# Optimization experiments

Hardware: AMD Instinct MI355X
Metric: run time of the kernel (lower is better)

The kernel has to match this reference:

```python
import jax, jax.numpy as jnp
import numpy as np

B, S, D, H = 2, 2048, 1024, 16
Dh = D // H
LN_EPS = 1e-5


def setup_inputs() -> dict:
    key = jax.random.key(0)
    ks = jax.random.split(key, 14)
    s = 1.0 / np.sqrt(D)
    return {
        "q": jax.random.normal(ks[0], (B, S, D), jnp.float32),
        "k": jax.random.normal(ks[1], (B, S, D), jnp.float32),
        "v": jax.random.normal(ks[2], (B, S, D), jnp.float32),
        "attn_mask": jax.random.randint(ks[3], (B, S, S), 0, 2).astype(bool),
        "Wq": jax.random.normal(ks[4], (D, D), jnp.float32) * s,
        "bq": jnp.zeros((D,), jnp.float32),
        "Wk": jax.random.normal(ks[5], (D, D), jnp.float32) * s,
        "bk": jnp.zeros((D,), jnp.float32),
        "Wv": jax.random.normal(ks[6], (D, D), jnp.float32) * s,
        "bv": jnp.zeros((D,), jnp.float32),
        "Wo": jax.random.normal(ks[7], (D, D), jnp.float32) * s,
        "bo": jnp.zeros((D,), jnp.float32),
        "gamma": jnp.ones((D,), jnp.float32),
        "beta": jnp.zeros((D,), jnp.float32),
    }


def reference(q, k, v, attn_mask, Wq, bq, Wk, bk, Wv, bv, Wo, bo, gamma, beta):
    residual = q
    # projections (W stored as [in, out])
    qh = (q @ Wq + bq).reshape(B, S, H, Dh).transpose(0, 2, 1, 3)  # [B,H,S,Dh]
    kh = (k @ Wk + bk).reshape(B, S, H, Dh).transpose(0, 2, 1, 3)
    vh = (v @ Wv + bv).reshape(B, S, H, Dh).transpose(0, 2, 1, 3)
    scores = jnp.einsum("bhqd,bhkd->bhqk", qh, kh) / np.sqrt(Dh)
    scores = jnp.where(attn_mask[:, None, :, :], -1e9, scores)
    attn = jax.nn.softmax(scores, axis=-1)  # dropout is identity in eval
    context = jnp.einsum("bhqk,bhkd->bhqd", attn, vh)  # [B,H,S,Dh]
    # faithful to original bug: flat reshape WITHOUT transposing heads back
    context = context.reshape(B, S, D)
    out = context @ Wo + bo
    x = residual + out
    mu = jnp.mean(x, axis=-1, keepdims=True)
    var = jnp.var(x, axis=-1, keepdims=True)
    out = (x - mu) / jnp.sqrt(var + LN_EPS) * gamma + beta
    return out, attn
```

## Files before the change

### kernel.cpp

```cpp
#include <hip/hip_runtime.h>
#include <hip/hip_bf16.h>

typedef __attribute__((ext_vector_type(8))) short bf16x8;
typedef __attribute__((ext_vector_type(4))) float f32x4;

__device__ __forceinline__ short f2bf(float f) {
    union { float f; unsigned u; } v; v.f = f;
    unsigned r = (v.u + 0x7FFFu + ((v.u >> 16) & 1u)) >> 16;
    return (short)r;
}
__device__ __forceinline__ float bf2f(short s) {
    union { unsigned u; float f; } v; v.u = ((unsigned)(unsigned short)s) << 16;
    return v.f;
}
__device__ __forceinline__ void gll16(const void* g, void* l) {
    __builtin_amdgcn_global_load_lds(
        (const __attribute__((address_space(1))) unsigned int*)g,
        (__attribute__((address_space(3))) unsigned int*)l, 16, 0, 0);
}

__global__ __launch_bounds__(256) void k_cvt(const float* __restrict__ in, short* __restrict__ out) {
    const long i = ((long)blockIdx.x * 256 + threadIdx.x) * 8;
    float4 f0 = *reinterpret_cast<const float4*>(&in[i]);
    float4 f1 = *reinterpret_cast<const float4*>(&in[i + 4]);
    bf16x8 v;
    v[0] = f2bf(f0.x); v[1] = f2bf(f0.y); v[2] = f2bf(f0.z); v[3] = f2bf(f0.w);
    v[4] = f2bf(f1.x); v[5] = f2bf(f1.y); v[6] = f2bf(f1.z); v[7] = f2bf(f1.w);
    *reinterpret_cast<bf16x8*>(&out[i]) = v;
}

__global__ __launch_bounds__(256) void k_wt(const float* __restrict__ W, short* __restrict__ WT) {
    __shared__ float t[32][33];
    const int rb = blockIdx.y * 32, cb = blockIdx.x * 32;
    const int tr = threadIdx.x >> 3, tc = (threadIdx.x & 7) * 4;
    const float4 v = *reinterpret_cast<const float4*>(&W[(long)(rb + tr) * 1024 + cb + tc]);
    t[tr][tc + 0] = v.x; t[tr][tc + 1] = v.y; t[tr][tc + 2] = v.z; t[tr][tc + 3] = v.w;
    __syncthreads();
    short4 o;
    o.x = f2bf(t[tc + 0][tr]); o.y = f2bf(t[tc + 1][tr]);
    o.z = f2bf(t[tc + 2][tr]); o.w = f2bf(t[tc + 3][tr]);
    *reinterpret_cast<short4*>(&WT[(long)(cb + tr) * 1024 + rb + tc]) = o;
}

__global__ __launch_bounds__(256) void k_mask_bits(const int* __restrict__ mask, unsigned* __restrict__ bits) {
    __shared__ int sm[8192];
    const long base = (long)blockIdx.x * 8192;
    const int tid = threadIdx.x;
#pragma unroll
    for (int i = 0; i < 8; ++i) {
        *reinterpret_cast<int4*>(&sm[i * 1024 + tid * 4]) =
            *reinterpret_cast<const int4*>(&mask[base + i * 1024 + tid * 4]);
    }
    __syncthreads();
    unsigned wv = 0;
#pragma unroll
    for (int j = 0; j < 32; ++j) wv |= (sm[tid * 32 + j] != 0 ? 1u : 0u) << j;
    bits[base / 32 + tid] = wv;
}

template<int MODE>
__global__ __launch_bounds__(256) void k_gemm2(
    const short* __restrict__ A, const short* __restrict__ BT,
    const float* __restrict__ bias, const float* __restrict__ resid,
    void* __restrict__ outp, float scale)
{
    __shared__ short As[128 * 64];
    __shared__ short Bs[128 * 64];
    const int tid = threadIdx.x, w = tid >> 6, lane = tid & 63;
    const int lr = lane & 15, lg = lane >> 4;
    const int rowbase = blockIdx.y * 128, colbase = blockIdx.x * 128;
    const int wr = (w >> 1) * 64, wc = (w & 1) * 64;
    const int srow = lane >> 3, sc_ = (lane & 7) ^ srow;

    f32x4 acc[4][4] = {};

    for (int kb = 0; kb < 1024; kb += 64) {
#pragma unroll
        for (int ii = 0; ii < 4; ++ii) {
            const int rl = w * 32 + ii * 8 + srow;
            gll16(A + (long)(rowbase + rl) * 1024 + kb + sc_ * 8, &As[(w * 32 + ii * 8) * 64]);
            gll16(BT + (long)(colbase + rl) * 1024 + kb + sc_ * 8, &Bs[(w * 32 + ii * 8) * 64]);
        }
        __syncthreads();
#pragma unroll
        for (int ks = 0; ks < 2; ++ks) {
            bf16x8 a[4], bq[4];
#pragma unroll
            for (int m = 0; m < 4; ++m) {
                const int r = wr + m * 16 + lr;
                a[m] = *reinterpret_cast<const bf16x8*>(&As[r * 64 + (((ks * 4 + lg) ^ (r & 7)) << 3)]);
            }
#pragma unroll
            for (int n = 0; n < 4; ++n) {
                const int r = wc + n * 16 + lr;
                bq[n] = *reinterpret_cast<const bf16x8*>(&Bs[r * 64 + (((ks * 4 + lg) ^ (r & 7)) << 3)]);
            }
#pragma unroll
            for (int m = 0; m < 4; ++m)
#pragma unroll
                for (int n = 0; n < 4; ++n)
                    acc[m][n] = __builtin_amdgcn_mfma_f32_16x16x32_bf16(a[m], bq[n], acc[m][n], 0, 0, 0);
        }
        __syncthreads();
    }

#pragma unroll
    for (int m = 0; m < 4; ++m) {
#pragma unroll
        for (int n = 0; n < 4; ++n) {
            const int C = colbase + wc + n * 16 + lr;
            const float bv = bias[C];
#pragma unroll
            for (int rr = 0; rr < 4; ++rr) {
                const int R = rowbase + wr + m * 16 + lg * 4 + rr;
                float val = (acc[m][n][rr] + bv) * scale;
                if (MODE == 0) {
                    const int b = R >> 11, s = R & 2047, h = C >> 6, dh = C & 63;
                    ((short*)outp)[(((long)(b * 16 + h) * 2048 + s) << 6) + dh] = f2bf(val);
                } else if (MODE == 1) {
                    const int b = R >> 11, s = R & 2047, h = C >> 6, dh = C & 63;
                    ((short*)outp)[(((long)(b * 16 + h) * 64 + dh) << 11) + s] = f2bf(val);
                } else {
                    const long idx = (long)R * 1024 + C;
                    ((float*)outp)[idx] = val + resid[idx];
                }
            }
        }
    }
}

__global__ __launch_bounds__(256) void k_attn(
    const short* __restrict__ qh, const short* __restrict__ kh,
    const short* __restrict__ vt, const unsigned* __restrict__ mbits,
    float* __restrict__ attn_out, short* __restrict__ ctxb)
{
    const int bh = blockIdx.y, b = bh >> 4;
    const int tid = threadIdx.x, w = tid >> 6, lane = tid & 63;
    const int lr = lane & 15, lg = lane >> 4;
    const int ibase = blockIdx.x * 64 + w * 16;

    __shared__ short Ks[64 * 64];
    __shared__ short Vs[64 * 64];
    __shared__ short Ps[4][16 * 72];

    const short* qhp = qh + ((long)bh * 2048 + ibase) * 64;
    const short* khp = kh + (long)bh * 2048 * 64;
    const short* vtp = vt + (long)bh * 64 * 2048;
    const unsigned* mbp = mbits + (long)b * 2048 * 64 + (long)ibase * 64;

    const bf16x8 aq0 = *reinterpret_cast<const bf16x8*>(&qhp[lr * 64 + lg * 8]);
    const bf16x8 aq1 = *reinterpret_cast<const bf16x8*>(&qhp[lr * 64 + 32 + lg * 8]);

    const int srow = lane >> 3, sc_ = (lane & 7) ^ srow;

    auto stage_k = [&](int ch) {
#pragma unroll
        for (int ii = 0; ii < 2; ++ii) {
            const int rl = w * 16 + ii * 8 + srow;
            gll16(khp + (long)(ch * 64 + rl) * 64 + sc_ * 8, &Ks[(w * 16 + ii * 8) * 64]);
        }
    };
    auto stage_v = [&](int ch) {
#pragma unroll
        for (int ii = 0; ii < 2; ++ii) {
            const int rl = w * 16 + ii * 8 + srow;
            gll16(vtp + (long)rl * 2048 + ch * 64 + sc_ * 8, &Vs[(w * 16 + ii * 8) * 64]);
        }
    };
    auto kfrag = [&](int t, int ks) -> bf16x8 {
        const int r = t * 16 + lr;
        return *reinterpret_cast<const bf16x8*>(&Ks[r * 64 + (((ks * 4 + lg) ^ (r & 7)) << 3)]);
    };
    auto vfrag = [&](int g, int ks) -> bf16x8 {
        const int r = g * 16 + lr;
        return *reinterpret_cast<const bf16x8*>(&Vs[r * 64 + (((ks * 4 + lg) ^ (r & 7)) << 3)]);
    };

    float ml[4], ll[4];
#pragma unroll
    for (int rr = 0; rr < 4; ++rr) { ml[rr] = -3.0e38f; ll[rr] = 0.f; }

    for (int ch = 0; ch < 32; ++ch) {
        stage_k(ch);
        __syncthreads();
        unsigned mw[4][2];
#pragma unroll
        for (int rr = 0; rr < 4; ++rr)
#pragma unroll
            for (int h = 0; h < 2; ++h)
                mw[rr][h] = mbp[(lg * 4 + rr) * 64 + ch * 2 + h];
#pragma unroll
        for (int t = 0; t < 4; ++t) {
            f32x4 sc = {};
            sc = __builtin_amdgcn_mfma_f32_16x16x32_bf16(aq0, kfrag(t, 0), sc, 0, 0, 0);
            sc = __builtin_amdgcn_mfma_f32_16x16x32_bf16(aq1, kfrag(t, 1), sc, 0, 0, 0);
#pragma unroll
            for (int rr = 0; rr < 4; ++rr) {
                const bool masked = (mw[rr][t >> 1] >> (((t & 1) << 4) + lr)) & 1;
                const float s = masked ? -1e9f : sc[rr];
                const float d = s - ml[rr];
                const float e = __expf(-fabsf(d));
                const bool gt = d > 0.f;
                ll[rr] = gt ? ll[rr] * e + 1.f : ll[rr] + e;
                ml[rr] = gt ? s : ml[rr];
            }
        }
        __syncthreads();
    }

    float mf[4], il[4];
#pragma unroll
    for (int rr = 0; rr < 4; ++rr) {
        float mx = ml[rr];
#pragma unroll
        for (int off = 1; off < 16; off <<= 1) mx = fmaxf(mx, __shfl_xor(mx, off, 16));
        float lw = ll[rr] * __expf(ml[rr] - mx);
#pragma unroll
        for (int off = 1; off < 16; off <<= 1) lw += __shfl_xor(lw, off, 16);
        mf[rr] = mx; il[rr] = 1.0f / lw;
    }

    f32x4 accc[4] = {};
    const long arow0 = (long)bh * 2048 + ibase;

    for (int ch = 0; ch < 32; ++ch) {
        stage_k(ch);
        stage_v(ch);
        __syncthreads();
        unsigned mw[4][2];
#pragma unroll
        for (int rr = 0; rr < 4; ++rr)
#pragma unroll
            for (int h = 0; h < 2; ++h)
                mw[rr][h] = mbp[(lg * 4 + rr) * 64 + ch * 2 + h];
#pragma unroll
        for (int t = 0; t < 4; ++t) {
            f32x4 sc = {};
            sc = __builtin_amdgcn_mfma_f32_16x16x32_bf16(aq0, kfrag(t, 0), sc, 0, 0, 0);
            sc = __builtin_amdgcn_mfma_f32_16x16x32_bf16(aq1, kfrag(t, 1), sc, 0, 0, 0);
#pragma unroll
            for (int rr = 0; rr < 4; ++rr) {
                const bool masked = (mw[rr][t >> 1] >> (((t & 1) << 4) + lr)) & 1;
                const float s = masked ? -1e9f : sc[rr];
                const float p = __expf(s - mf[rr]) * il[rr];
                Ps[w][(lg * 4 + rr) * 72 + t * 16 + lr] = f2bf(p);
            }
        }
#pragma unroll
        for (int ks = 0; ks < 2; ++ks) {
            const bf16x8 pa = *reinterpret_cast<const bf16x8*>(&Ps[w][lr * 72 + ks * 32 + lg * 8]);
#pragma unroll
            for (int g = 0; g < 4; ++g)
                accc[g] = __builtin_amdgcn_mfma_f32_16x16x32_bf16(pa, vfrag(g, ks), accc[g], 0, 0, 0);
        }
#pragma unroll
        for (int i2 = 0; i2 < 4; ++i2) {
            const int r = i2 * 4 + lg;
            const short4 p4 = *reinterpret_cast<const short4*>(&Ps[w][r * 72 + lr * 4]);
            float4 o;
            o.x = bf2f(p4.x); o.y = bf2f(p4.y); o.z = bf2f(p4.z); o.w = bf2f(p4.w);
            *reinterpret_cast<float4*>(&attn_out[(arow0 + r) * 2048 + ch * 64 + lr * 4]) = o;
        }
        __syncthreads();
    }

#pragma unroll
    for (int g = 0; g < 4; ++g)
#pragma unroll
        for (int rr = 0; rr < 4; ++rr)
            ctxb[(arow0 + lg * 4 + rr) * 64 + g * 16 + lr] = f2bf(accc[g][rr]);
}

__global__ __launch_bounds__(256) void k_ln(const float* __restrict__ x,
    const float* __restrict__ gamma, const float* __restrict__ beta,
    float* __restrict__ out)
{
    __shared__ float red[8];
    const int r = blockIdx.x, tid = threadIdx.x;
    const float4 v = reinterpret_cast<const float4*>(x + (long)r * 1024)[tid];
    float s = v.x + v.y + v.z + v.w;
    float q2 = v.x * v.x + v.y * v.y + v.z * v.z + v.w * v.w;
#pragma unroll
    for (int off = 32; off; off >>= 1) {
        s += __shfl_xor(s, off, 64);
        q2 += __shfl_xor(q2, off, 64);
    }
    if ((tid & 63) == 0) { red[(tid >> 6) * 2] = s; red[(tid >> 6) * 2 + 1] = q2; }
    __syncthreads();
    s = red[0] + red[2] + red[4] + red[6];
    q2 = red[1] + red[3] + red[5] + red[7];
    const float mu = s * (1.0f / 1024.0f);
    const float var = q2 * (1.0f / 1024.0f) - mu * mu;
    const float rs = rsqrtf(var + 1e-5f);
    const float4 g = reinterpret_cast<const float4*>(gamma)[tid];
    const float4 bb = reinterpret_cast<const float4*>(beta)[tid];
    float4 o;
    o.x = (v.x - mu) * rs * g.x + bb.x;
    o.y = (v.y - mu) * rs * g.y + bb.y;
    o.z = (v.z - mu) * rs * g.z + bb.z;
    o.w = (v.w - mu) * rs * g.w + bb.w;
    reinterpret_cast<float4*>(out + (long)r * 1024)[tid] = o;
}

extern "C" void kernel_launch(void* const* d_in, const int* in_sizes, int n_in,
                              void* d_out, int out_size, void* d_ws, size_t ws_size,
                              hipStream_t stream)
{
    const float* qin  = (const float*)d_in[0];
    const float* kin  = (const float*)d_in[1];
    const float* vin  = (const float*)d_in[2];
    const int*   mask = (const int*)d_in[3];
    const float* Wq = (const float*)d_in[4];
    const float* bq = (const float*)d_in[5];
    const float* Wk = (const float*)d_in[6];
    const float* bk = (const float*)d_in[7];
    const float* Wv = (const float*)d_in[8];
    const float* bv = (const float*)d_in[9];
    const float* Wo = (const float*)d_in[10];
    const float* bo = (const float*)d_in[11];
    const float* gamma = (const float*)d_in[12];
    const float* beta  = (const float*)d_in[13];

    char* ws = (char*)d_ws;
    short* WqT = (short*)(ws + (0ul  << 20));
    short* WkT = (short*)(ws + (2ul  << 20));
    short* WvT = (short*)(ws + (4ul  << 20));
    short* WoT = (short*)(ws + (6ul  << 20));
    short* qbf = (short*)(ws + (8ul  << 20));
    short* kbf = (short*)(ws + (16ul << 20));
    short* vbf = (short*)(ws + (24ul << 20));
    short* qh  = (short*)(ws + (32ul << 20));
    short* khb = (short*)(ws + (40ul << 20));
    short* vtb = (short*)(ws + (48ul << 20));
    unsigned* mb = (unsigned*)(ws + (56ul << 20));
    short* ctxb = (short*)(ws + (57ul << 20));
    float* xb   = (float*)(ws + (8ul  << 20));

    float* outLN = (float*)d_out;
    float* attnO = (float*)d_out + 4194304;

    const dim3 blk(256);
    k_cvt<<<dim3(2048), blk, 0, stream>>>(qin, qbf);
    k_cvt<<<dim3(2048), blk, 0, stream>>>(kin, kbf);
    k_cvt<<<dim3(2048), blk, 0, stream>>>(vin, vbf);
    k_wt<<<dim3(32, 32), blk, 0, stream>>>(Wq, WqT);
    k_wt<<<dim3(32, 32), blk, 0, stream>>>(Wk, WkT);
    k_wt<<<dim3(32, 32), blk, 0, stream>>>(Wv, WvT);
    k_wt<<<dim3(32, 32), blk, 0, stream>>>(Wo, WoT);
    k_mask_bits<<<dim3(1024), blk, 0, stream>>>(mask, mb);

    const dim3 gg(8, 32);
    k_gemm2<0><<<gg, blk, 0, stream>>>(qbf, WqT, bq, nullptr, qh,  0.125f);
    k_gemm2<0><<<gg, blk, 0, stream>>>(kbf, WkT, bk, nullptr, khb, 1.0f);
    k_gemm2<1><<<gg, blk, 0, stream>>>(vbf, WvT, bv, nullptr, vtb, 1.0f);

    k_attn<<<dim3(32, 32), blk, 0, stream>>>(qh, khb, vtb, mb, attnO, ctxb);

    k_gemm2<2><<<gg, blk, 0, stream>>>(ctxb, WoT, bo, qin, xb, 1.0f);
    k_ln<<<dim3(4096), blk, 0, stream>>>(xb, gamma, beta, outLN);
}
```

Before: 365.6 us.

## Merge prep launches, batch QKV GEMMs, and split attention keys across waves

Measured after the change: 433.6 us. 1.19x slower.

```diff
diff --git a/kernel.cpp b/kernel.cpp
--- a/kernel.cpp
+++ b/kernel.cpp
@@ -19,50 +19,132 @@
         (__attribute__((address_space(3))) unsigned int*)l, 16, 0, 0);
 }
 
-__global__ __launch_bounds__(256) void k_cvt(const float* __restrict__ in, short* __restrict__ out) {
-    const long i = ((long)blockIdx.x * 256 + threadIdx.x) * 8;
-    float4 f0 = *reinterpret_cast<const float4*>(&in[i]);
-    float4 f1 = *reinterpret_cast<const float4*>(&in[i + 4]);
-    bf16x8 v;
-    v[0] = f2bf(f0.x); v[1] = f2bf(f0.y); v[2] = f2bf(f0.z); v[3] = f2bf(f0.w);
-    v[4] = f2bf(f1.x); v[5] = f2bf(f1.y); v[6] = f2bf(f1.z); v[7] = f2bf(f1.w);
-    *reinterpret_cast<bf16x8*>(&out[i]) = v;
-}
-
-__global__ __launch_bounds__(256) void k_wt(const float* __restrict__ W, short* __restrict__ WT) {
-    __shared__ float t[32][33];
-    const int rb = blockIdx.y * 32, cb = blockIdx.x * 32;
-    const int tr = threadIdx.x >> 3, tc = (threadIdx.x & 7) * 4;
-    const float4 v = *reinterpret_cast<const float4*>(&W[(long)(rb + tr) * 1024 + cb + tc]);
-    t[tr][tc + 0] = v.x; t[tr][tc + 1] = v.y; t[tr][tc + 2] = v.z; t[tr][tc + 3] = v.w;
-    __syncthreads();
-    short4 o;
-    o.x = f2bf(t[tc + 0][tr]); o.y = f2bf(t[tc + 1][tr]);
-    o.z = f2bf(t[tc + 2][tr]); o.w = f2bf(t[tc + 3][tr]);
-    *reinterpret_cast<short4*>(&WT[(long)(cb + tr) * 1024 + rb + tc]) = o;
-}
-
-__global__ __launch_bounds__(256) void k_mask_bits(const int* __restrict__ mask, unsigned* __restrict__ bits) {
+__global__ __launch_bounds__(256) void k_prep(
+    const float* __restrict__ qin, const float* __restrict__ kin, const float* __restrict__ vin,
+    short* __restrict__ qbf, short* __restrict__ kbf, short* __restrict__ vbf,
+    const float* __restrict__ Wq, const float* __restrict__ Wk,
+    const float* __restrict__ Wv, const float* __restrict__ Wo,
+    short* __restrict__ WqT, short* __restrict__ WkT,
+    short* __restrict__ WvT, short* __restrict__ WoT,
+    const int* __restrict__ mask, unsigned* __restrict__ mb)
+{
     __shared__ int sm[8192];
-    const long base = (long)blockIdx.x * 8192;
-    const int tid = threadIdx.x;
-#pragma unroll
-    for (int i = 0; i < 8; ++i) {
-        *reinterpret_cast<int4*>(&sm[i * 1024 + tid * 4]) =
-            *reinterpret_cast<const int4*>(&mask[base + i * 1024 + tid * 4]);
-    }
-    __syncthreads();
-    unsigned wv = 0;
-#pragma unroll
-    for (int j = 0; j < 32; ++j) wv |= (sm[tid * 32 + j] != 0 ? 1u : 0u) << j;
-    bits[base / 32 + tid] = wv;
-}
-
-template<int MODE>
-__global__ __launch_bounds__(256) void k_gemm2(
+    const int bid = blockIdx.x, tid = threadIdx.x;
+    if (bid < 6144) {
+        const float* in = bid < 2048 ? qin : (bid < 4096 ? kin : vin);
+        short* out = bid < 2048 ? qbf : (bid < 4096 ? kbf : vbf);
+        const long i = ((long)(bid & 2047) * 256 + tid) * 8;
+        float4 f0 = *reinterpret_cast<const float4*>(&in[i]);
+        float4 f1 = *reinterpret_cast<const float4*>(&in[i + 4]);
+        bf16x8 v;
+        v[0] = f2bf(f0.x); v[1] = f2bf(f0.y); v[2] = f2bf(f0.z); v[3] = f2bf(f0.w);
+        v[4] = f2bf(f1.x); v[5] = f2bf(f1.y); v[6] = f2bf(f1.z); v[7] = f2bf(f1.w);
+        *reinterpret_cast<bf16x8*>(&out[i]) = v;
+    } else if (bid < 10240) {
+        const int t2 = bid - 6144, which = t2 >> 10, local = t2 & 1023;
+        const float* W = which == 0 ? Wq : (which == 1 ? Wk : (which == 2 ? Wv : Wo));
+        short* WT = which == 0 ? WqT : (which == 1 ? WkT : (which == 2 ? WvT : WoT));
+        float (*t)[33] = reinterpret_cast<float(*)[33]>(sm);
+        const int rb = (local >> 5) * 32, cb = (local & 31) * 32;
+        const int tr = tid >> 3, tc = (tid & 7) * 4;
+        const float4 v = *reinterpret_cast<const float4*>(&W[(long)(rb + tr) * 1024 + cb + tc]);
+        t[tr][tc + 0] = v.x; t[tr][tc + 1] = v.y; t[tr][tc + 2] = v.z; t[tr][tc + 3] = v.w;
+        __syncthreads();
+        short4 o;
+        o.x = f2bf(t[tc + 0][tr]); o.y = f2bf(t[tc + 1][tr]);
+        o.z = f2bf(t[tc + 2][tr]); o.w = f2bf(t[tc + 3][tr]);
+        *reinterpret_cast<short4*>(&WT[(long)(cb + tr) * 1024 + rb + tc]) = o;
+    } else {
+        const long base = (long)(bid - 10240) * 8192;
+#pragma unroll
+        for (int i = 0; i < 8; ++i)
+            *reinterpret_cast<int4*>(&sm[i * 1024 + tid * 4]) =
+                *reinterpret_cast<const int4*>(&mask[base + i * 1024 + tid * 4]);
+        __syncthreads();
+        unsigned wv = 0;
+#pragma unroll
+        for (int j = 0; j < 32; ++j) wv |= (sm[tid * 32 + j] != 0 ? 1u : 0u) << j;
+        mb[base / 32 + tid] = wv;
+    }
+}
+
+__global__ __launch_bounds__(256) void k_gemm_qkv(
+    const short* __restrict__ A0, const short* __restrict__ A1, const short* __restrict__ A2,
+    const short* __restrict__ B0, const short* __restrict__ B1, const short* __restrict__ B2,
+    const float* __restrict__ b0, const float* __restrict__ b1, const float* __restrict__ b2,
+    short* __restrict__ o0, short* __restrict__ o1, short* __restrict__ o2)
+{
+    __shared__ short As[128 * 64];
+    __shared__ short Bs[128 * 64];
+    const int z = blockIdx.z;
+    const short* A = z == 0 ? A0 : (z == 1 ? A1 : A2);
+    const short* BT = z == 0 ? B0 : (z == 1 ? B1 : B2);
+    const float* bias = z == 0 ? b0 : (z == 1 ? b1 : b2);
+    short* outp = z == 0 ? o0 : (z == 1 ? o1 : o2);
+    const float scale = z == 0 ? 0.125f : 1.0f;
+
+    const int tid = threadIdx.x, w = tid >> 6, lane = tid & 63;
+    const int lr = lane & 15, lg = lane >> 4;
+    const int rowbase = blockIdx.y * 128, colbase = blockIdx.x * 128;
+    const int wr = (w >> 1) * 64, wc = (w & 1) * 64;
+    const int srow = lane >> 3, sc_ = (lane & 7) ^ srow;
+
+    f32x4 acc[4][4] = {};
+
+    for (int kb = 0; kb < 1024; kb += 64) {
+#pragma unroll
+        for (int ii = 0; ii < 4; ++ii) {
+            const int rl = w * 32 + ii * 8 + srow;
+            gll16(A + (long)(rowbase + rl) * 1024 + kb + sc_ * 8, &As[(w * 32 + ii * 8) * 64]);
+            gll16(BT + (long)(colbase + rl) * 1024 + kb + sc_ * 8, &Bs[(w * 32 + ii * 8) * 64]);
+        }
+        __syncthreads();
+#pragma unroll
+        for (int ks = 0; ks < 2; ++ks) {
+            bf16x8 a[4], bq[4];
+#pragma unroll
+            for (int m = 0; m < 4; ++m) {
+                const int r = wr + m * 16 + lr;
+                a[m] = *reinterpret_cast<const bf16x8*>(&As[r * 64 + (((ks * 4 + lg) ^ (r & 7)) << 3)]);
+            }
+#pragma unroll
+            for (int n = 0; n < 4; ++n) {
+                const int r = wc + n * 16 + lr;
+                bq[n] = *reinterpret_cast<const bf16x8*>(&Bs[r * 64 + (((ks * 4 + lg) ^ (r & 7)) << 3)]);
+            }
+#pragma unroll
+            for (int m = 0; m < 4; ++m)
+#pragma unroll
+                for (int n = 0; n < 4; ++n)
+                    acc[m][n] = __builtin_amdgcn_mfma_f32_16x16x32_bf16(a[m], bq[n], acc[m][n], 0, 0, 0);
+        }
+        __syncthreads();
+    }
+
+#pragma unroll
+    for (int m = 0; m < 4; ++m) {
+#pragma unroll
+        for (int n = 0; n < 4; ++n) {
+            const int C = colbase + wc + n * 16 + lr;
+            const float bv = bias[C];
+#pragma unroll
+            for (int rr = 0; rr < 4; ++rr) {
+                const int R = rowbase + wr + m * 16 + lg * 4 + rr;
+                const float val = (acc[m][n][rr] + bv) * scale;
+                const int b = R >> 11, s = R & 2047, h = C >> 6, dh = C & 63;
+                if (z != 2)
+                    outp[(((long)(b * 16 + h) * 2048 + s) << 6) + dh] = f2bf(val);
+                else
+                    outp[(((long)(b * 16 + h) * 64 + dh) << 11) + s] = f2bf(val);
+            }
+        }
+    }
+}
+
+__global__ __launch_bounds__(256) void k_gemm_o(
     const short* __restrict__ A, const short* __restrict__ BT,
     const float* __restrict__ bias, const float* __restrict__ resid,
-    void* __restrict__ outp, float scale)
+    float* __restrict__ outp)
 {
     __shared__ short As[128 * 64];
     __shared__ short Bs[128 * 64];
@@ -113,35 +195,30 @@
 #pragma unroll
             for (int rr = 0; rr < 4; ++rr) {
                 const int R = rowbase + wr + m * 16 + lg * 4 + rr;
-                float val = (acc[m][n][rr] + bv) * scale;
-                if (MODE == 0) {
-                    const int b = R >> 11, s = R & 2047, h = C >> 6, dh = C & 63;
-                    ((short*)outp)[(((long)(b * 16 + h) * 2048 + s) << 6) + dh] = f2bf(val);
-                } else if (MODE == 1) {
-                    const int b = R >> 11, s = R & 2047, h = C >> 6, dh = C & 63;
-                    ((short*)outp)[(((long)(b * 16 + h) * 64 + dh) << 11) + s] = f2bf(val);
-                } else {
-                    const long idx = (long)R * 1024 + C;
-                    ((float*)outp)[idx] = val + resid[idx];
-                }
-            }
-        }
-    }
-}
-
-__global__ __launch_bounds__(256) void k_attn(
+                const long idx = (long)R * 1024 + C;
+                outp[idx] = acc[m][n][rr] + bv + resid[idx];
+            }
+        }
+    }
+}
+
+__global__ __launch_bounds__(256, 2) void k_attn(
     const short* __restrict__ qh, const short* __restrict__ kh,
     const short* __restrict__ vt, const unsigned* __restrict__ mbits,
     float* __restrict__ attn_out, short* __restrict__ ctxb)
 {
-    const int bh = blockIdx.y, b = bh >> 4;
+    const int g = blockIdx.x, xcd = g & 7, idx = g >> 3;
+    const int bh = idx >> 4, qtile = xcd * 16 + (idx & 15);
+    const int b = bh >> 4;
     const int tid = threadIdx.x, w = tid >> 6, lane = tid & 63;
     const int lr = lane & 15, lg = lane >> 4;
-    const int ibase = blockIdx.x * 64 + w * 16;
-
-    __shared__ short Ks[64 * 64];
-    __shared__ short Vs[64 * 64];
+    const int ibase = qtile * 16;
+    const int jb0 = w * 512;
+
     __shared__ short Ps[4][16 * 72];
+    __shared__ float cred[4][16][64];
+    __shared__ float redm[4][16];
+    __shared__ float redl[4][16];
 
     const short* qhp = qh + ((long)bh * 2048 + ibase) * 64;
     const short* khp = kh + (long)bh * 2048 * 64;
@@ -151,107 +228,105 @@
     const bf16x8 aq0 = *reinterpret_cast<const bf16x8*>(&qhp[lr * 64 + lg * 8]);
     const bf16x8 aq1 = *reinterpret_cast<const bf16x8*>(&qhp[lr * 64 + 32 + lg * 8]);
 
-    const int srow = lane >> 3, sc_ = (lane & 7) ^ srow;
-
-    auto stage_k = [&](int ch) {
-#pragma unroll
-        for (int ii = 0; ii < 2; ++ii) {
-            const int rl = w * 16 + ii * 8 + srow;
-            gll16(khp + (long)(ch * 64 + rl) * 64 + sc_ * 8, &Ks[(w * 16 + ii * 8) * 64]);
-        }
-    };
-    auto stage_v = [&](int ch) {
-#pragma unroll
-        for (int ii = 0; ii < 2; ++ii) {
-            const int rl = w * 16 + ii * 8 + srow;
-            gll16(vtp + (long)rl * 2048 + ch * 64 + sc_ * 8, &Vs[(w * 16 + ii * 8) * 64]);
-        }
-    };
-    auto kfrag = [&](int t, int ks) -> bf16x8 {
-        const int r = t * 16 + lr;
-        return *reinterpret_cast<const bf16x8*>(&Ks[r * 64 + (((ks * 4 + lg) ^ (r & 7)) << 3)]);
-    };
-    auto vfrag = [&](int g, int ks) -> bf16x8 {
-        const int r = g * 16 + lr;
-        return *reinterpret_cast<const bf16x8*>(&Vs[r * 64 + (((ks * 4 + lg) ^ (r & 7)) << 3)]);
-    };
-
-    float ml[4], ll[4];
-#pragma unroll
-    for (int rr = 0; rr < 4; ++rr) { ml[rr] = -3.0e38f; ll[rr] = 0.f; }
-
-    for (int ch = 0; ch < 32; ++ch) {
-        stage_k(ch);
-        __syncthreads();
+    f32x4 st[32];
+#pragma unroll
+    for (int ch = 0; ch < 8; ++ch) {
+        const short* kc = khp + (long)(jb0 + ch * 64) * 64;
+        bf16x8 kf[8];
+#pragma unroll
+        for (int t = 0; t < 4; ++t) {
+#pragma unroll
+            for (int ks = 0; ks < 2; ++ks)
+                kf[t * 2 + ks] = *reinterpret_cast<const bf16x8*>(&kc[(t * 16 + lr) * 64 + ks * 32 + lg * 8]);
+        }
         unsigned mw[4][2];
 #pragma unroll
         for (int rr = 0; rr < 4; ++rr)
 #pragma unroll
             for (int h = 0; h < 2; ++h)
-                mw[rr][h] = mbp[(lg * 4 + rr) * 64 + ch * 2 + h];
+                mw[rr][h] = mbp[(lg * 4 + rr) * 64 + (jb0 >> 5) + ch * 2 + h];
 #pragma unroll
         for (int t = 0; t < 4; ++t) {
             f32x4 sc = {};
-            sc = __builtin_amdgcn_mfma_f32_16x16x32_bf16(aq0, kfrag(t, 0), sc, 0, 0, 0);
-            sc = __builtin_amdgcn_mfma_f32_16x16x32_bf16(aq1, kfrag(t, 1), sc, 0, 0, 0);
+            sc = __builtin_amdgcn_mfma_f32_16x16x32_bf16(aq0, kf[t * 2], sc, 0, 0, 0);
+            sc = __builtin_amdgcn_mfma_f32_16x16x32_bf16(aq1, kf[t * 2 + 1], sc, 0, 0, 0);
 #pragma unroll
             for (int rr = 0; rr < 4; ++rr) {
                 const bool masked = (mw[rr][t >> 1] >> (((t & 1) << 4) + lr)) & 1;
-                const float s = masked ? -1e9f : sc[rr];
-                const float d = s - ml[rr];
-                const float e = __expf(-fabsf(d));
-                const bool gt = d > 0.f;
-                ll[rr] = gt ? ll[rr] * e + 1.f : ll[rr] + e;
-                ml[rr] = gt ? s : ml[rr];
-            }
-        }
-        __syncthreads();
-    }
-
-    float mf[4], il[4];
+                st[ch * 4 + t][rr] = masked ? -1e9f : sc[rr];
+            }
+        }
+    }
+
+    float mloc[4];
 #pragma unroll
     for (int rr = 0; rr < 4; ++rr) {
-        float mx = ml[rr];
-#pragma unroll
-        for (int off = 1; off < 16; off <<= 1) mx = fmaxf(mx, __shfl_xor(mx, off, 16));
-        float lw = ll[rr] * __expf(ml[rr] - mx);
-#pragma unroll
-        for (int off = 1; off < 16; off <<= 1) lw += __shfl_xor(lw, off, 16);
-        mf[rr] = mx; il[rr] = 1.0f / lw;
-    }
-
-    f32x4 accc[4] = {};
+        float m = st[0][rr];
+#pragma unroll
+        for (int ct = 1; ct < 32; ++ct) m = fmaxf(m, st[ct][rr]);
+#pragma unroll
+        for (int off = 1; off < 16; off <<= 1) m = fmaxf(m, __shfl_xor(m, off, 16));
+        mloc[rr] = m;
+    }
+    if (lr == 0) {
+#pragma unroll
+        for (int rr = 0; rr < 4; ++rr) redm[w][lg * 4 + rr] = mloc[rr];
+    }
+    __syncthreads();
+    float mf[4];
+#pragma unroll
+    for (int rr = 0; rr < 4; ++rr) {
+        const int row = lg * 4 + rr;
+        mf[rr] = fmaxf(fmaxf(redm[0][row], redm[1][row]), fmaxf(redm[2][row], redm[3][row]));
+    }
+    float lloc[4] = {0.f, 0.f, 0.f, 0.f};
+#pragma unroll
+    for (int ct = 0; ct < 32; ++ct) {
+#pragma unroll
+        for (int rr = 0; rr < 4; ++rr) {
+            const float e = __expf(st[ct][rr] - mf[rr]);
+            st[ct][rr] = e;
+            lloc[rr] += e;
+        }
+    }
+#pragma unroll
+    for (int rr = 0; rr < 4; ++rr) {
+#pragma unroll
+        for (int off = 1; off < 16; off <<= 1) lloc[rr] += __shfl_xor(lloc[rr], off, 16);
+    }
+    if (lr == 0) {
+#pragma unroll
+        for (int rr = 0; rr < 4; ++rr) redl[w][lg * 4 + rr] = lloc[rr];
+    }
+    __syncthreads();
+    float il[4];
+#pragma unroll
+    for (int rr = 0; rr < 4; ++rr) {
+        const int row = lg * 4 + rr;
+        il[rr] = 1.0f / (redl[0][row] + redl[1][row] + redl[2][row] + redl[3][row]);
+    }
+
+    f32x4 acc[4] = {};
     const long arow0 = (long)bh * 2048 + ibase;
-
-    for (int ch = 0; ch < 32; ++ch) {
-        stage_k(ch);
-        stage_v(ch);
-        __syncthreads();
-        unsigned mw[4][2];
-#pragma unroll
-        for (int rr = 0; rr < 4; ++rr)
-#pragma unroll
-            for (int h = 0; h < 2; ++h)
-                mw[rr][h] = mbp[(lg * 4 + rr) * 64 + ch * 2 + h];
-#pragma unroll
-        for (int t = 0; t < 4; ++t) {
-            f32x4 sc = {};
-            sc = __builtin_amdgcn_mfma_f32_16x16x32_bf16(aq0, kfrag(t, 0), sc, 0, 0, 0);
-            sc = __builtin_amdgcn_mfma_f32_16x16x32_bf16(aq1, kfrag(t, 1), sc, 0, 0, 0);
-#pragma unroll
-            for (int rr = 0; rr < 4; ++rr) {
-                const bool masked = (mw[rr][t >> 1] >> (((t & 1) << 4) + lr)) & 1;
-                const float s = masked ? -1e9f : sc[rr];
-                const float p = __expf(s - mf[rr]) * il[rr];
-                Ps[w][(lg * 4 + rr) * 72 + t * 16 + lr] = f2bf(p);
-            }
-        }
-#pragma unroll
-        for (int ks = 0; ks < 2; ++ks) {
-            const bf16x8 pa = *reinterpret_cast<const bf16x8*>(&Ps[w][lr * 72 + ks * 32 + lg * 8]);
-#pragma unroll
-            for (int g = 0; g < 4; ++g)
-                accc[g] = __builtin_amdgcn_mfma_f32_16x16x32_bf16(pa, vfrag(g, ks), accc[g], 0, 0, 0);
+#pragma unroll
+    for (int ch = 0; ch < 8; ++ch) {
+#pragma unroll
+        for (int t = 0; t < 4; ++t)
+#pragma unroll
+            for (int rr = 0; rr < 4; ++rr)
+                Ps[w][(lg * 4 + rr) * 72 + t * 16 + lr] = f2bf(st[ch * 4 + t][rr] * il[rr]);
+        const short* vc = vtp + jb0 + ch * 64;
+        bf16x8 pa[2];
+#pragma unroll
+        for (int ks = 0; ks < 2; ++ks)
+            pa[ks] = *reinterpret_cast<const bf16x8*>(&Ps[w][lr * 72 + ks * 32 + lg * 8]);
+#pragma unroll
+        for (int g4 = 0; g4 < 4; ++g4) {
+#pragma unroll
+            for (int ks = 0; ks < 2; ++ks) {
+                const bf16x8 vf = *reinterpret_cast<const bf16x8*>(&vc[(long)(g4 * 16 + lr) * 2048 + ks * 32 + lg * 8]);
+                acc[g4] = __builtin_amdgcn_mfma_f32_16x16x32_bf16(pa[ks], vf, acc[g4], 0, 0, 0);
+            }
         }
 #pragma unroll
         for (int i2 = 0; i2 < 4; ++i2) {
@@ -259,16 +334,29 @@
             const short4 p4 = *reinterpret_cast<const short4*>(&Ps[w][r * 72 + lr * 4]);
             float4 o;
             o.x = bf2f(p4.x); o.y = bf2f(p4.y); o.z = bf2f(p4.z); o.w = bf2f(p4.w);
-            *reinterpret_cast<float4*>(&attn_out[(arow0 + r) * 2048 + ch * 64 + lr * 4]) = o;
-        }
-        __syncthreads();
-    }
-
-#pragma unroll
-    for (int g = 0; g < 4; ++g)
+            *reinterpret_cast<float4*>(&attn_out[(arow0 + r) * 2048 + jb0 + ch * 64 + lr * 4]) = o;
+        }
+    }
+
+#pragma unroll
+    for (int g4 = 0; g4 < 4; ++g4)
 #pragma unroll
         for (int rr = 0; rr < 4; ++rr)
-            ctxb[(arow0 + lg * 4 + rr) * 64 + g * 16 + lr] = f2bf(accc[g][rr]);
+            cred[w][lg * 4 + rr][g4 * 16 + lr] = acc[g4][rr];
+    __syncthreads();
+    {
+        const int e = tid * 4, row = e >> 6, col = e & 63;
+        float4 s0 = *reinterpret_cast<const float4*>(&cred[0][row][col]);
+        float4 s1 = *reinterpret_cast<const float4*>(&cred[1][row][col]);
+        float4 s2 = *reinterpret_cast<const float4*>(&cred[2][row][col]);
+        float4 s3 = *reinterpret_cast<const float4*>(&cred[3][row][col]);
+        short4 o;
+        o.x = f2bf(s0.x + s1.x + s2.x + s3.x);
+        o.y = f2bf(s0.y + s1.y + s2.y + s3.y);
+        o.z = f2bf(s0.z + s1.z + s2.z + s3.z);
+        o.w = f2bf(s0.w + s1.w + s2.w + s3.w);
+        *reinterpret_cast<short4*>(&ctxb[(arow0 + row) * 64 + col]) = o;
+    }
 }
 
 __global__ __launch_bounds__(256) void k_ln(const float* __restrict__ x,
@@ -340,22 +428,11 @@
     float* attnO = (float*)d_out + 4194304;
 
     const dim3 blk(256);
-    k_cvt<<<dim3(2048), blk, 0, stream>>>(qin, qbf);
-    k_cvt<<<dim3(2048), blk, 0, stream>>>(kin, kbf);
-    k_cvt<<<dim3(2048), blk, 0, stream>>>(vin, vbf);
-    k_wt<<<dim3(32, 32), blk, 0, stream>>>(Wq, WqT);
-    k_wt<<<dim3(32, 32), blk, 0, stream>>>(Wk, WkT);
-    k_wt<<<dim3(32, 32), blk, 0, stream>>>(Wv, WvT);
-    k_wt<<<dim3(32, 32), blk, 0, stream>>>(Wo, WoT);
-    k_mask_bits<<<dim3(1024), blk, 0, stream>>>(mask, mb);
-
-    const dim3 gg(8, 32);
-    k_gemm2<0><<<gg, blk, 0, stream>>>(qbf, WqT, bq, nullptr, qh,  0.125f);
-    k_gemm2<0><<<gg, blk, 0, stream>>>(kbf, WkT, bk, nullptr, khb, 1.0f);
-    k_gemm2<1><<<gg, blk, 0, stream>>>(vbf, WvT, bv, nullptr, vtb, 1.0f);
-
-    k_attn<<<dim3(32, 32), blk, 0, stream>>>(qh, khb, vtb, mb, attnO, ctxb);
-
-    k_gemm2<2><<<gg, blk, 0, stream>>>(ctxb, WoT, bo, qin, xb, 1.0f);
+    k_prep<<<dim3(11264), blk, 0, stream>>>(qin, kin, vin, qbf, kbf, vbf,
+                                            Wq, Wk, Wv, Wo, WqT, WkT, WvT, WoT, mask, mb);
+    k_gemm_qkv<<<dim3(8, 32, 3), blk, 0, stream>>>(qbf, kbf, vbf, WqT, WkT, WvT,
+                                                   bq, bk, bv, qh, khb, vtb);
+    k_attn<<<dim3(4096), blk, 0, stream>>>(qh, khb, vtb, mb, attnO, ctxb);
+    k_gemm_o<<<dim3(8, 32), blk, 0, stream>>>(ctxb, WoT, bo, qin, xb);
     k_ln<<<dim3(4096), blk, 0, stream>>>(xb, gamma, beta, outLN);
 }
```
